# Optimization experiments

Measured on AMD Instinct MI355X. Metric: run time of the kernel, lower is better.

Reference implementation:

```python
import jax, jax.numpy as jnp
import numpy as np

N_NODES = 100000
N_EDGES = 1600000
D_IN = 128
D_OUT = 128
EPS = 1e-12  # torch F.normalize default eps


def setup_inputs() -> dict:
    key = jax.random.key(0)
    k1, k2, k3, k4, k5 = jax.random.split(key, 5)
    features = jax.random.normal(k1, (N_NODES, D_IN), dtype=jnp.float32)
    edge_src = jax.random.randint(k2, (N_EDGES,), 0, N_NODES, dtype=jnp.int64)
    edge_dst = jax.random.randint(k3, (N_EDGES,), 0, N_NODES, dtype=jnp.int64)
    node_mask = jnp.ones((N_NODES,), dtype=bool)
    W = jax.random.normal(k4, (D_OUT, D_IN), dtype=jnp.float32) * (1.0 / np.sqrt(D_IN))
    b = jax.random.normal(k5, (D_OUT,), dtype=jnp.float32) * 0.01
    return {"features": features, "edge_src": edge_src, "edge_dst": edge_dst,
            "node_mask": node_mask, "W": W, "b": b}


def reference(features, edge_src, edge_dst, node_mask, W, b):
    # Message passing: sum neighbor (src) features into each dst node.
    msgs = features[edge_src]                                   # [E, D_IN]
    agg = jax.ops.segment_sum(msgs, edge_dst, num_segments=features.shape[0])  # [N, D_IN]
    # Active nodes: h_N[node] = features[node] + sum(neighbors); inactive keep features.
    h_N = jnp.where(node_mask[:, None], features + agg, features)
    # F.normalize(h_N, dim=1): L2 normalize rows with eps clamp.
    norm = jnp.linalg.norm(h_N, axis=1, keepdims=True)
    h_norm = h_N / jnp.maximum(norm, EPS)
    # Linear layer.
    return h_norm @ W.T + b
```

## Files before the change

### kernel.cpp

```cpp
#include <hip/hip_runtime.h>

#define N_NODES 100000
#define D 128
#define N_EDGES 1600000
#define NBINS 3125
#define BCAP 1024
#define NCB 49
#define CCAP 40960
#define EPB1 1000
#define SLICE 2048
#define NSLICE 20
#define AST 136
#define LCAP 64
#define LST 68

typedef unsigned short u16;
typedef __attribute__((ext_vector_type(8))) short short8;
typedef __attribute__((ext_vector_type(8))) unsigned short ushort8;
typedef __attribute__((ext_vector_type(4))) float f32x4;

__device__ __forceinline__ u16 f2bf(float f) {
    union { float f; unsigned int i; } c;
    c.f = f;
    unsigned int r = c.i + 0x7FFFu + ((c.i >> 16) & 1u);
    return (u16)(r >> 16);
}

__device__ __forceinline__ void bf16_acc8(unsigned int u, float* a) {
    union { unsigned int i; float f; } c;
    c.i = u << 16;          a[0] += c.f;
    c.i = u & 0xffff0000u;  a[1] += c.f;
}

__global__ __launch_bounds__(256) void conv_all(const float* __restrict__ feat,
                                                const float* __restrict__ Wg,
                                                u16* __restrict__ featb,
                                                u16* __restrict__ Wbf,
                                                int* __restrict__ gcnt) {
    const int b = blockIdx.x, t = threadIdx.x;
    if (b < 6250) {
        if (!featb) return;
        int idx = (b * 256 + t) * 8;
        f32x4 v0 = *(const f32x4*)(feat + idx);
        f32x4 v1 = *(const f32x4*)(feat + idx + 4);
        ushort8 o;
        o[0] = f2bf(v0.x); o[1] = f2bf(v0.y); o[2] = f2bf(v0.z); o[3] = f2bf(v0.w);
        o[4] = f2bf(v1.x); o[5] = f2bf(v1.y); o[6] = f2bf(v1.z); o[7] = f2bf(v1.w);
        *(ushort8*)(featb + idx) = o;
    } else if (b < 6258) {
        int idx = ((b - 6250) * 256 + t) * 8;
        f32x4 v0 = *(const f32x4*)(Wg + idx);
        f32x4 v1 = *(const f32x4*)(Wg + idx + 4);
        ushort8 o;
        o[0] = f2bf(v0.x); o[1] = f2bf(v0.y); o[2] = f2bf(v0.z); o[3] = f2bf(v0.w);
        o[4] = f2bf(v1.x); o[5] = f2bf(v1.y); o[6] = f2bf(v1.z); o[7] = f2bf(v1.w);
        *(ushort8*)(Wbf + idx) = o;
    } else {
        int i = (b - 6258) * 256 + t;
        if (i < 3328) gcnt[i] = 0;
    }
}

__global__ __launch_bounds__(256) void coarse_bin(const int* __restrict__ esrc,
                                                  const int* __restrict__ edst,
                                                  int* __restrict__ gcnt,
                                                  int2* __restrict__ cpool) {
    __shared__ int2 stash[EPB1];
    __shared__ int hist[NCB];
    __shared__ int hbase[NCB];
    const int t = threadIdx.x;
    const int base = blockIdx.x * EPB1;

    if (t < NCB) hist[t] = 0;
    __syncthreads();
    for (int i = t; i < EPB1; i += 256) {
        int s = esrc[base + i];
        int d0 = edst[base + i];
        stash[i] = make_int2(s, d0);
        atomicAdd(&hist[d0 >> 11], 1);
    }
    __syncthreads();
    if (t < NCB) {
        int h = hist[t];
        hbase[t] = h ? atomicAdd(gcnt + 3136 + t, h) : 0;
        hist[t] = 0;
    }
    __syncthreads();
    for (int i = t; i < EPB1; i += 256) {
        int2 p = stash[i];
        int c = p.y >> 11;
        int r = atomicAdd(&hist[c], 1);
        int pos = hbase[c] + r;
        if (pos < CCAP) cpool[c * CCAP + pos] = p;
    }
}

__global__ __launch_bounds__(256) void fine_bin(int* __restrict__ gcnt,
                                                const int2* __restrict__ cpool,
                                                unsigned* __restrict__ pool) {
    __shared__ unsigned stash[SLICE];
    __shared__ unsigned char fwb[SLICE];
    __shared__ int hist[64];
    __shared__ int hbase[64];
    const int t = threadIdx.x;
    const int cb = blockIdx.x / NSLICE;
    const int sl = blockIdx.x % NSLICE;

    int cnt = gcnt[3136 + cb];
    if (cnt > CCAP) cnt = CCAP;
    int ne = cnt - sl * SLICE;
    if (ne <= 0) return;
    if (ne > SLICE) ne = SLICE;

    if (t < 64) hist[t] = 0;
    __syncthreads();
    const int2* seg = cpool + cb * CCAP + sl * SLICE;
    for (int i = t; i < ne; i += 256) {
        int2 p = seg[i];
        unsigned fw = ((unsigned)p.y >> 5) & 63u;
        stash[i] = ((unsigned)(p.y & 31) << 17) | (unsigned)p.x;
        fwb[i] = (unsigned char)fw;
        atomicAdd(&hist[fw], 1);
    }
    __syncthreads();
    if (t < 64) {
        int h = hist[t];
        hbase[t] = h ? atomicAdd(gcnt + cb * 64 + t, h) : 0;
        hist[t] = 0;
    }
    __syncthreads();
    for (int i = t; i < ne; i += 256) {
        int fw = fwb[i];
        int r = atomicAdd(&hist[fw], 1);
        int pos = hbase[fw] + r;
        if (pos < BCAP) pool[(size_t)(cb * 64 + fw) * BCAP + pos] = stash[i];
    }
}

template<bool BF16FEAT>
__global__ __launch_bounds__(256) void fused_gnl(const void* __restrict__ featv,
                                                 const int* __restrict__ gcnt,
                                                 const unsigned* __restrict__ pool,
                                                 const u16* __restrict__ Wbf,
                                                 const float* __restrict__ bg,
                                                 float* __restrict__ out) {
    __shared__ u16 Al[32 * AST];
    __shared__ int lists[32 * LST];
    __shared__ int lcnt[32];
    const int t = threadIdx.x;
    const int nbase = blockIdx.x * 32;
    const int nl = t >> 3;
    const int g = t & 7;
    const int n = nbase + nl;

    {
        int ne = gcnt[blockIdx.x];
        if (ne > BCAP) ne = BCAP;
        if (t < 32) lcnt[t] = 0;
        __syncthreads();
        const unsigned* seg = pool + (size_t)blockIdx.x * BCAP;
        for (int i = t; i < ne; i += 256) {
            unsigned p = seg[i];
            unsigned rel = p >> 17;
            int r = atomicAdd(&lcnt[rel], 1);
            if (r < LCAP) lists[rel * LST + r] = (int)(p & 0x1FFFFu);
        }
        __syncthreads();
    }

    float acc[16];
    if (BF16FEAT) {
        const u16* fb = (const u16*)featv + (size_t)n * D + g * 16;
        uint4 p0 = *(const uint4*)(fb);
        uint4 p1 = *(const uint4*)(fb + 8);
        #pragma unroll
        for (int k = 0; k < 16; k++) acc[k] = 0.f;
        bf16_acc8(p0.x, acc + 0);  bf16_acc8(p0.y, acc + 2);
        bf16_acc8(p0.z, acc + 4);  bf16_acc8(p0.w, acc + 6);
        bf16_acc8(p1.x, acc + 8);  bf16_acc8(p1.y, acc + 10);
        bf16_acc8(p1.z, acc + 12); bf16_acc8(p1.w, acc + 14);
    } else {
        const float* ff = (const float*)featv + (size_t)n * D + g * 16;
        f32x4 v0 = *(const f32x4*)(ff);
        f32x4 v1 = *(const f32x4*)(ff + 4);
        f32x4 v2 = *(const f32x4*)(ff + 8);
        f32x4 v3 = *(const f32x4*)(ff + 12);
        acc[0]=v0.x; acc[1]=v0.y; acc[2]=v0.z; acc[3]=v0.w;
        acc[4]=v1.x; acc[5]=v1.y; acc[6]=v1.z; acc[7]=v1.w;
        acc[8]=v2.x; acc[9]=v2.y; acc[10]=v2.z; acc[11]=v2.w;
        acc[12]=v3.x; acc[13]=v3.y; acc[14]=v3.z; acc[15]=v3.w;
    }

    int deg = lcnt[nl];
    if (deg > LCAP) deg = LCAP;
    const int* bk = lists + nl * LST;
    int e = 0;
    if (BF16FEAT) {
        const u16* fb = (const u16*)featv;
        for (; e + 4 <= deg; e += 4) {
            int4 s4 = *(const int4*)(bk + e);
            const u16* r0 = fb + (size_t)s4.x * D + g * 16;
            const u16* r1 = fb + (size_t)s4.y * D + g * 16;
            const u16* r2 = fb + (size_t)s4.z * D + g * 16;
            const u16* r3 = fb + (size_t)s4.w * D + g * 16;
            uint4 a0 = *(const uint4*)(r0), b0 = *(const uint4*)(r0 + 8);
            uint4 a1 = *(const uint4*)(r1), b1 = *(const uint4*)(r1 + 8);
            uint4 a2 = *(const uint4*)(r2), b2 = *(const uint4*)(r2 + 8);
            uint4 a3 = *(const uint4*)(r3), b3 = *(const uint4*)(r3 + 8);
            bf16_acc8(a0.x, acc+0); bf16_acc8(a0.y, acc+2); bf16_acc8(a0.z, acc+4); bf16_acc8(a0.w, acc+6);
            bf16_acc8(b0.x, acc+8); bf16_acc8(b0.y, acc+10); bf16_acc8(b0.z, acc+12); bf16_acc8(b0.w, acc+14);
            bf16_acc8(a1.x, acc+0); bf16_acc8(a1.y, acc+2); bf16_acc8(a1.z, acc+4); bf16_acc8(a1.w, acc+6);
            bf16_acc8(b1.x, acc+8); bf16_acc8(b1.y, acc+10); bf16_acc8(b1.z, acc+12); bf16_acc8(b1.w, acc+14);
            bf16_acc8(a2.x, acc+0); bf16_acc8(a2.y, acc+2); bf16_acc8(a2.z, acc+4); bf16_acc8(a2.w, acc+6);
            bf16_acc8(b2.x, acc+8); bf16_acc8(b2.y, acc+10); bf16_acc8(b2.z, acc+12); bf16_acc8(b2.w, acc+14);
            bf16_acc8(a3.x, acc+0); bf16_acc8(a3.y, acc+2); bf16_acc8(a3.z, acc+4); bf16_acc8(a3.w, acc+6);
            bf16_acc8(b3.x, acc+8); bf16_acc8(b3.y, acc+10); bf16_acc8(b3.z, acc+12); bf16_acc8(b3.w, acc+14);
        }
        for (; e < deg; e++) {
            const u16* r0 = fb + (size_t)bk[e] * D + g * 16;
            uint4 a0 = *(const uint4*)(r0), b0 = *(const uint4*)(r0 + 8);
            bf16_acc8(a0.x, acc+0); bf16_acc8(a0.y, acc+2); bf16_acc8(a0.z, acc+4); bf16_acc8(a0.w, acc+6);
            bf16_acc8(b0.x, acc+8); bf16_acc8(b0.y, acc+10); bf16_acc8(b0.z, acc+12); bf16_acc8(b0.w, acc+14);
        }
    } else {
        const float* ff = (const float*)featv;
        for (; e + 2 <= deg; e += 2) {
            int2 s2 = *(const int2*)(bk + e);
            const float* r0 = ff + (size_t)s2.x * D + g * 16;
            const float* r1 = ff + (size_t)s2.y * D + g * 16;
            f32x4 x0 = *(const f32x4*)(r0),     x1 = *(const f32x4*)(r0 + 4);
            f32x4 x2 = *(const f32x4*)(r0 + 8), x3 = *(const f32x4*)(r0 + 12);
            f32x4 y0 = *(const f32x4*)(r1),     y1 = *(const f32x4*)(r1 + 4);
            f32x4 y2 = *(const f32x4*)(r1 + 8), y3 = *(const f32x4*)(r1 + 12);
            acc[0]+=x0.x+y0.x; acc[1]+=x0.y+y0.y; acc[2]+=x0.z+y0.z; acc[3]+=x0.w+y0.w;
            acc[4]+=x1.x+y1.x; acc[5]+=x1.y+y1.y; acc[6]+=x1.z+y1.z; acc[7]+=x1.w+y1.w;
            acc[8]+=x2.x+y2.x; acc[9]+=x2.y+y2.y; acc[10]+=x2.z+y2.z; acc[11]+=x2.w+y2.w;
            acc[12]+=x3.x+y3.x; acc[13]+=x3.y+y3.y; acc[14]+=x3.z+y3.z; acc[15]+=x3.w+y3.w;
        }
        for (; e < deg; e++) {
            const float* r0 = ff + (size_t)bk[e] * D + g * 16;
            f32x4 x0 = *(const f32x4*)(r0),     x1 = *(const f32x4*)(r0 + 4);
            f32x4 x2 = *(const f32x4*)(r0 + 8), x3 = *(const f32x4*)(r0 + 12);
            acc[0]+=x0.x; acc[1]+=x0.y; acc[2]+=x0.z; acc[3]+=x0.w;
            acc[4]+=x1.x; acc[5]+=x1.y; acc[6]+=x1.z; acc[7]+=x1.w;
            acc[8]+=x2.x; acc[9]+=x2.y; acc[10]+=x2.z; acc[11]+=x2.w;
            acc[12]+=x3.x; acc[13]+=x3.y; acc[14]+=x3.z; acc[15]+=x3.w;
        }
    }

    float ss = 0.f;
    #pragma unroll
    for (int k = 0; k < 16; k++) ss += acc[k] * acc[k];
    #pragma unroll
    for (int off = 4; off; off >>= 1) ss += __shfl_xor(ss, off, 8);
    const float inv = 1.0f / fmaxf(sqrtf(ss), 1e-12f);

    {
        ushort8 o0, o1;
        o0[0]=f2bf(acc[0]*inv); o0[1]=f2bf(acc[1]*inv); o0[2]=f2bf(acc[2]*inv); o0[3]=f2bf(acc[3]*inv);
        o0[4]=f2bf(acc[4]*inv); o0[5]=f2bf(acc[5]*inv); o0[6]=f2bf(acc[6]*inv); o0[7]=f2bf(acc[7]*inv);
        o1[0]=f2bf(acc[8]*inv); o1[1]=f2bf(acc[9]*inv); o1[2]=f2bf(acc[10]*inv); o1[3]=f2bf(acc[11]*inv);
        o1[4]=f2bf(acc[12]*inv); o1[5]=f2bf(acc[13]*inv); o1[6]=f2bf(acc[14]*inv); o1[7]=f2bf(acc[15]*inv);
        u16* dst = Al + nl * AST + g * 16;
        *(ushort8*)(dst)     = o0;
        *(ushort8*)(dst + 8) = o1;
    }
    __syncthreads();

    const int w = t >> 6, lane = t & 63;
    const int mb = (w >> 1) * 16, nb = (w & 1) * 64;
    const int quad = lane >> 4, r = lane & 15;
    f32x4 c0 = {0,0,0,0}, c1 = {0,0,0,0}, c2 = {0,0,0,0}, c3 = {0,0,0,0};
    #pragma unroll
    for (int kt = 0; kt < 4; kt++) {
        const int ko = kt * 32 + quad * 8;
        short8 a  = *(const short8*)(Al + (mb + r) * AST + ko);
        short8 b0 = *(const short8*)(Wbf + (nb +  0 + r) * D + ko);
        short8 b1 = *(const short8*)(Wbf + (nb + 16 + r) * D + ko);
        short8 b2 = *(const short8*)(Wbf + (nb + 32 + r) * D + ko);
        short8 b3 = *(const short8*)(Wbf + (nb + 48 + r) * D + ko);
        c0 = __builtin_amdgcn_mfma_f32_16x16x32_bf16(a, b0, c0, 0, 0, 0);
        c1 = __builtin_amdgcn_mfma_f32_16x16x32_bf16(a, b1, c1, 0, 0, 0);
        c2 = __builtin_amdgcn_mfma_f32_16x16x32_bf16(a, b2, c2, 0, 0, 0);
        c3 = __builtin_amdgcn_mfma_f32_16x16x32_bf16(a, b3, c3, 0, 0, 0);
    }

    {
        const float bb0 = bg[nb + r], bb1 = bg[nb + 16 + r];
        const float bb2 = bg[nb + 32 + r], bb3 = bg[nb + 48 + r];
        float* outb = out + (size_t)(nbase + mb + quad * 4) * D;
        #pragma unroll
        for (int reg = 0; reg < 4; reg++) {
            float* rowp = outb + reg * D + nb + r;
            rowp[0]  = c0[reg] + bb0;
            rowp[16] = c1[reg] + bb1;
            rowp[32] = c2[reg] + bb2;
            rowp[48] = c3[reg] + bb3;
        }
    }
}

__global__ __launch_bounds__(256) void scatter(const float* __restrict__ feat,
                                               const int* __restrict__ esrc,
                                               const int* __restrict__ edst,
                                               float* __restrict__ agg) {
    int gid = blockIdx.x * 256 + threadIdx.x;
    int e = gid >> 5;
    int q = (gid & 31) << 2;
    int s = esrc[e];
    int d0 = edst[e];
    const float4 a = *(const float4*)(feat + s * D + q);
    float* dst = agg + d0 * D + q;
    unsafeAtomicAdd(dst + 0, a.x);
    unsafeAtomicAdd(dst + 1, a.y);
    unsafeAtomicAdd(dst + 2, a.z);
    unsafeAtomicAdd(dst + 3, a.w);
}

__global__ __launch_bounds__(256) void norm_linear_mfma(const float* __restrict__ Wg,
                                                        const float* __restrict__ bg,
                                                        float* __restrict__ out) {
    __shared__ u16 Wl[128 * AST];
    __shared__ u16 Al[32 * AST];
    __shared__ float bl[128];
    const int t = threadIdx.x;
    const int nbase = blockIdx.x * 32;

    for (int idx = t * 8; idx < 128 * 128; idx += 256 * 8) {
        int row = idx >> 7, col = idx & 127;
        f32x4 v0 = *(const f32x4*)(Wg + idx);
        f32x4 v1 = *(const f32x4*)(Wg + idx + 4);
        u16* dst = Wl + row * AST + col;
        dst[0] = f2bf(v0.x); dst[1] = f2bf(v0.y); dst[2] = f2bf(v0.z); dst[3] = f2bf(v0.w);
        dst[4] = f2bf(v1.x); dst[5] = f2bf(v1.y); dst[6] = f2bf(v1.z); dst[7] = f2bf(v1.w);
    }
    if (t < 128) bl[t] = bg[t];
    {
        const int n = t >> 3, seg = t & 7;
        const float* src = out + (nbase + n) * D + seg * 16;
        f32x4 v0 = *(const f32x4*)(src);
        f32x4 v1 = *(const f32x4*)(src + 4);
        f32x4 v2 = *(const f32x4*)(src + 8);
        f32x4 v3 = *(const f32x4*)(src + 12);
        float ss = v0.x*v0.x + v0.y*v0.y + v0.z*v0.z + v0.w*v0.w
                 + v1.x*v1.x + v1.y*v1.y + v1.z*v1.z + v1.w*v1.w
                 + v2.x*v2.x + v2.y*v2.y + v2.z*v2.z + v2.w*v2.w
                 + v3.x*v3.x + v3.y*v3.y + v3.z*v3.z + v3.w*v3.w;
        #pragma unroll
        for (int off = 4; off; off >>= 1) ss += __shfl_xor(ss, off, 8);
        const float inv = 1.0f / fmaxf(sqrtf(ss), 1e-12f);
        u16* dst = Al + n * AST + seg * 16;
        dst[0]  = f2bf(v0.x * inv); dst[1]  = f2bf(v0.y * inv);
        dst[2]  = f2bf(v0.z * inv); dst[3]  = f2bf(v0.w * inv);
        dst[4]  = f2bf(v1.x * inv); dst[5]  = f2bf(v1.y * inv);
        dst[6]  = f2bf(v1.z * inv); dst[7]  = f2bf(v1.w * inv);
        dst[8]  = f2bf(v2.x * inv); dst[9]  = f2bf(v2.y * inv);
        dst[10] = f2bf(v2.z * inv); dst[11] = f2bf(v2.w * inv);
        dst[12] = f2bf(v3.x * inv); dst[13] = f2bf(v3.y * inv);
        dst[14] = f2bf(v3.z * inv); dst[15] = f2bf(v3.w * inv);
    }
    __syncthreads();

    const int w = t >> 6, lane = t & 63;
    const int mb = (w >> 1) * 16, nb = (w & 1) * 64;
    const int quad = lane >> 4, r = lane & 15;
    f32x4 c0 = {0,0,0,0}, c1 = {0,0,0,0}, c2 = {0,0,0,0}, c3 = {0,0,0,0};
    #pragma unroll
    for (int kt = 0; kt < 4; kt++) {
        const int ko = kt * 32 + quad * 8;
        short8 a = *(const short8*)(Al + (mb + r) * AST + ko);
        short8 b0 = *(const short8*)(Wl + (nb +  0 + r) * AST + ko);
        short8 b1 = *(const short8*)(Wl + (nb + 16 + r) * AST + ko);
        short8 b2 = *(const short8*)(Wl + (nb + 32 + r) * AST + ko);
        short8 b3 = *(const short8*)(Wl + (nb + 48 + r) * AST + ko);
        c0 = __builtin_amdgcn_mfma_f32_16x16x32_bf16(a, b0, c0, 0, 0, 0);
        c1 = __builtin_amdgcn_mfma_f32_16x16x32_bf16(a, b1, c1, 0, 0, 0);
        c2 = __builtin_amdgcn_mfma_f32_16x16x32_bf16(a, b2, c2, 0, 0, 0);
        c3 = __builtin_amdgcn_mfma_f32_16x16x32_bf16(a, b3, c3, 0, 0, 0);
    }
    {
        float* outb = out + (nbase + mb + quad * 4) * D;
        const float bb0 = bl[nb + r], bb1 = bl[nb + 16 + r];
        const float bb2 = bl[nb + 32 + r], bb3 = bl[nb + 48 + r];
        #pragma unroll
        for (int reg = 0; reg < 4; reg++) {
            float* rowp = outb + reg * D + nb + r;
            rowp[0]  = c0[reg] + bb0;
            rowp[16] = c1[reg] + bb1;
            rowp[32] = c2[reg] + bb2;
            rowp[48] = c3[reg] + bb3;
        }
    }
}

extern "C" void kernel_launch(void* const* d_in, const int* in_sizes, int n_in,
                              void* d_out, int out_size, void* d_ws, size_t ws_size,
                              hipStream_t stream) {
    const float* feat = (const float*)d_in[0];
    const int*   esrc = (const int*)d_in[1];
    const int*   edst = (const int*)d_in[2];
    const float* W = (const float*)d_in[n_in - 2];
    const float* b = (const float*)d_in[n_in - 1];
    float* out = (float*)d_out;

    const long poolw = (long)NBINS * BCAP;
    const long need_f32  = 3328 + 8192 + poolw;
    const long need_bf16 = need_f32 + 6400000;
    const long availw = (long)(ws_size / 4);

    if (availw >= need_f32) {
        const bool bf16feat = (availw >= need_bf16);
        int* gcnt = (int*)d_ws;
        u16* Wbf = (u16*)(gcnt + 3328);
        unsigned* pool = (unsigned*)(Wbf + 16384);
        u16* featb = bf16feat ? (u16*)(pool + poolw) : (u16*)nullptr;
        int2* cpool = (int2*)d_out;

        conv_all<<<6271, 256, 0, stream>>>(feat, W, featb, Wbf, gcnt);
        coarse_bin<<<N_EDGES / EPB1, 256, 0, stream>>>(esrc, edst, gcnt, cpool);
        fine_bin<<<NCB * NSLICE, 256, 0, stream>>>(gcnt, cpool, pool);
        if (bf16feat)
            fused_gnl<true><<<NBINS, 256, 0, stream>>>(featb, gcnt, pool, Wbf, b, out);
        else
            fused_gnl<false><<<NBINS, 256, 0, stream>>>(feat, gcnt, pool, Wbf, b, out);
    } else {
        hipMemcpyAsync(out, feat, (size_t)N_NODES * D * sizeof(float),
                       hipMemcpyDeviceToDevice, stream);
        scatter<<<(N_EDGES * 32) / 256, 256, 0, stream>>>(feat, esrc, edst, out);
        norm_linear_mfma<<<N_NODES / 32, 256, 0, stream>>>(W, b, out);
    }
}
```

Baseline: 235.1 us.

## Halve fused-kernel node tile to 16 and split neighbor gather across thread pairs

The fused gather/normalize/linear kernel now handles 16 nodes per block instead of 32. Each node gets 16 threads, with two threads splitting the neighbor quads and combining their partial sums through a shuffle. Fine binning goes to 128 bins per coarse bin with a bucket capacity of 512, and coarse_bin first sorts edges locally in shared memory so its global writes are contiguous. The aim is more blocks and more memory-level parallelism in the gather, and better coalescing in binning. The cost is an extra shuffle reduction, a smaller MFMA tile per block, and W fragments being reloaded by twice as many blocks.

```diff
diff --git a/kernel.cpp b/kernel.cpp
--- a/kernel.cpp
+++ b/kernel.cpp
@@ -3,8 +3,9 @@
 #define N_NODES 100000
 #define D 128
 #define N_EDGES 1600000
-#define NBINS 3125
-#define BCAP 1024
+#define NBINS 6250
+#define BCAP 512
+#define NFINW 6272
 #define NCB 49
 #define CCAP 40960
 #define EPB1 1000
@@ -57,7 +58,7 @@
         *(ushort8*)(Wbf + idx) = o;
     } else {
         int i = (b - 6258) * 256 + t;
-        if (i < 3328) gcnt[i] = 0;
+        if (i < 6400) gcnt[i] = 0;
     }
 }
 
@@ -66,8 +67,10 @@
                                                   int* __restrict__ gcnt,
                                                   int2* __restrict__ cpool) {
     __shared__ int2 stash[EPB1];
+    __shared__ int2 sorted[EPB1];
     __shared__ int hist[NCB];
     __shared__ int hbase[NCB];
+    __shared__ int loff[NCB];
     const int t = threadIdx.x;
     const int base = blockIdx.x * EPB1;
 
@@ -80,9 +83,14 @@
         atomicAdd(&hist[d0 >> 11], 1);
     }
     __syncthreads();
+    if (t == 0) {
+        int run = 0;
+        for (int c = 0; c < NCB; c++) { loff[c] = run; run += hist[c]; }
+    }
+    __syncthreads();
     if (t < NCB) {
         int h = hist[t];
-        hbase[t] = h ? atomicAdd(gcnt + 3136 + t, h) : 0;
+        hbase[t] = h ? atomicAdd(gcnt + NFINW + t, h) : 0;
         hist[t] = 0;
     }
     __syncthreads();
@@ -90,7 +98,13 @@
         int2 p = stash[i];
         int c = p.y >> 11;
         int r = atomicAdd(&hist[c], 1);
-        int pos = hbase[c] + r;
+        sorted[loff[c] + r] = p;
+    }
+    __syncthreads();
+    for (int i = t; i < EPB1; i += 256) {
+        int2 p = sorted[i];
+        int c = p.y >> 11;
+        int pos = hbase[c] + (i - loff[c]);
         if (pos < CCAP) cpool[c * CCAP + pos] = p;
     }
 }
@@ -100,32 +114,32 @@
                                                 unsigned* __restrict__ pool) {
     __shared__ unsigned stash[SLICE];
     __shared__ unsigned char fwb[SLICE];
-    __shared__ int hist[64];
-    __shared__ int hbase[64];
+    __shared__ int hist[128];
+    __shared__ int hbase[128];
     const int t = threadIdx.x;
     const int cb = blockIdx.x / NSLICE;
     const int sl = blockIdx.x % NSLICE;
 
-    int cnt = gcnt[3136 + cb];
+    int cnt = gcnt[NFINW + cb];
     if (cnt > CCAP) cnt = CCAP;
     int ne = cnt - sl * SLICE;
     if (ne <= 0) return;
     if (ne > SLICE) ne = SLICE;
 
-    if (t < 64) hist[t] = 0;
+    if (t < 128) hist[t] = 0;
     __syncthreads();
     const int2* seg = cpool + cb * CCAP + sl * SLICE;
     for (int i = t; i < ne; i += 256) {
         int2 p = seg[i];
-        unsigned fw = ((unsigned)p.y >> 5) & 63u;
-        stash[i] = ((unsigned)(p.y & 31) << 17) | (unsigned)p.x;
+        unsigned fw = ((unsigned)p.y >> 4) & 127u;
+        stash[i] = ((unsigned)(p.y & 15) << 17) | (unsigned)p.x;
         fwb[i] = (unsigned char)fw;
         atomicAdd(&hist[fw], 1);
     }
     __syncthreads();
-    if (t < 64) {
+    if (t < 128) {
         int h = hist[t];
-        hbase[t] = h ? atomicAdd(gcnt + cb * 64 + t, h) : 0;
+        hbase[t] = h ? atomicAdd(gcnt + cb * 128 + t, h) : 0;
         hist[t] = 0;
     }
     __syncthreads();
@@ -133,7 +147,7 @@
         int fw = fwb[i];
         int r = atomicAdd(&hist[fw], 1);
         int pos = hbase[fw] + r;
-        if (pos < BCAP) pool[(size_t)(cb * 64 + fw) * BCAP + pos] = stash[i];
+        if (pos < BCAP) pool[(size_t)(cb * 128 + fw) * BCAP + pos] = stash[i];
     }
 }
 
@@ -144,19 +158,20 @@
                                                  const u16* __restrict__ Wbf,
                                                  const float* __restrict__ bg,
                                                  float* __restrict__ out) {
-    __shared__ u16 Al[32 * AST];
-    __shared__ int lists[32 * LST];
-    __shared__ int lcnt[32];
+    __shared__ u16 Al[16 * AST];
+    __shared__ int lists[16 * LST];
+    __shared__ int lcnt[16];
     const int t = threadIdx.x;
-    const int nbase = blockIdx.x * 32;
-    const int nl = t >> 3;
-    const int g = t & 7;
+    const int nbase = blockIdx.x * 16;
+    const int nl = t >> 4;
+    const int g = (t >> 1) & 7;
+    const int h = t & 1;
     const int n = nbase + nl;
 
     {
         int ne = gcnt[blockIdx.x];
         if (ne > BCAP) ne = BCAP;
-        if (t < 32) lcnt[t] = 0;
+        if (t < 16) lcnt[t] = 0;
         __syncthreads();
         const unsigned* seg = pool + (size_t)blockIdx.x * BCAP;
         for (int i = t; i < ne; i += 256) {
@@ -169,36 +184,40 @@
     }
 
     float acc[16];
+    #pragma unroll
+    for (int k = 0; k < 16; k++) acc[k] = 0.f;
     if (BF16FEAT) {
-        const u16* fb = (const u16*)featv + (size_t)n * D + g * 16;
-        uint4 p0 = *(const uint4*)(fb);
-        uint4 p1 = *(const uint4*)(fb + 8);
-        #pragma unroll
-        for (int k = 0; k < 16; k++) acc[k] = 0.f;
-        bf16_acc8(p0.x, acc + 0);  bf16_acc8(p0.y, acc + 2);
-        bf16_acc8(p0.z, acc + 4);  bf16_acc8(p0.w, acc + 6);
-        bf16_acc8(p1.x, acc + 8);  bf16_acc8(p1.y, acc + 10);
-        bf16_acc8(p1.z, acc + 12); bf16_acc8(p1.w, acc + 14);
+        if (h == 0) {
+            const u16* fr = (const u16*)featv + (size_t)n * D + g * 16;
+            uint4 p0 = *(const uint4*)(fr);
+            uint4 p1 = *(const uint4*)(fr + 8);
+            bf16_acc8(p0.x, acc + 0);  bf16_acc8(p0.y, acc + 2);
+            bf16_acc8(p0.z, acc + 4);  bf16_acc8(p0.w, acc + 6);
+            bf16_acc8(p1.x, acc + 8);  bf16_acc8(p1.y, acc + 10);
+            bf16_acc8(p1.z, acc + 12); bf16_acc8(p1.w, acc + 14);
+        }
     } else {
-        const float* ff = (const float*)featv + (size_t)n * D + g * 16;
-        f32x4 v0 = *(const f32x4*)(ff);
-        f32x4 v1 = *(const f32x4*)(ff + 4);
-        f32x4 v2 = *(const f32x4*)(ff + 8);
-        f32x4 v3 = *(const f32x4*)(ff + 12);
-        acc[0]=v0.x; acc[1]=v0.y; acc[2]=v0.z; acc[3]=v0.w;
-        acc[4]=v1.x; acc[5]=v1.y; acc[6]=v1.z; acc[7]=v1.w;
-        acc[8]=v2.x; acc[9]=v2.y; acc[10]=v2.z; acc[11]=v2.w;
-        acc[12]=v3.x; acc[13]=v3.y; acc[14]=v3.z; acc[15]=v3.w;
+        if (h == 0) {
+            const float* ff = (const float*)featv + (size_t)n * D + g * 16;
+            f32x4 v0 = *(const f32x4*)(ff);
+            f32x4 v1 = *(const f32x4*)(ff + 4);
+            f32x4 v2 = *(const f32x4*)(ff + 8);
+            f32x4 v3 = *(const f32x4*)(ff + 12);
+            acc[0]=v0.x; acc[1]=v0.y; acc[2]=v0.z; acc[3]=v0.w;
+            acc[4]=v1.x; acc[5]=v1.y; acc[6]=v1.z; acc[7]=v1.w;
+            acc[8]=v2.x; acc[9]=v2.y; acc[10]=v2.z; acc[11]=v2.w;
+            acc[12]=v3.x; acc[13]=v3.y; acc[14]=v3.z; acc[15]=v3.w;
+        }
     }
 
     int deg = lcnt[nl];
     if (deg > LCAP) deg = LCAP;
     const int* bk = lists + nl * LST;
-    int e = 0;
+    const int m4 = deg >> 2;
     if (BF16FEAT) {
         const u16* fb = (const u16*)featv;
-        for (; e + 4 <= deg; e += 4) {
-            int4 s4 = *(const int4*)(bk + e);
+        for (int q = h; q < m4; q += 2) {
+            int4 s4 = *(const int4*)(bk + q * 4);
             const u16* r0 = fb + (size_t)s4.x * D + g * 16;
             const u16* r1 = fb + (size_t)s4.y * D + g * 16;
             const u16* r2 = fb + (size_t)s4.z * D + g * 16;
@@ -216,46 +235,55 @@
             bf16_acc8(a3.x, acc+0); bf16_acc8(a3.y, acc+2); bf16_acc8(a3.z, acc+4); bf16_acc8(a3.w, acc+6);
             bf16_acc8(b3.x, acc+8); bf16_acc8(b3.y, acc+10); bf16_acc8(b3.z, acc+12); bf16_acc8(b3.w, acc+14);
         }
-        for (; e < deg; e++) {
-            const u16* r0 = fb + (size_t)bk[e] * D + g * 16;
-            uint4 a0 = *(const uint4*)(r0), b0 = *(const uint4*)(r0 + 8);
-            bf16_acc8(a0.x, acc+0); bf16_acc8(a0.y, acc+2); bf16_acc8(a0.z, acc+4); bf16_acc8(a0.w, acc+6);
-            bf16_acc8(b0.x, acc+8); bf16_acc8(b0.y, acc+10); bf16_acc8(b0.z, acc+12); bf16_acc8(b0.w, acc+14);
+        if (h == (m4 & 1)) {
+            for (int e = m4 * 4; e < deg; e++) {
+                const u16* r0 = fb + (size_t)bk[e] * D + g * 16;
+                uint4 a0 = *(const uint4*)(r0), b0 = *(const uint4*)(r0 + 8);
+                bf16_acc8(a0.x, acc+0); bf16_acc8(a0.y, acc+2); bf16_acc8(a0.z, acc+4); bf16_acc8(a0.w, acc+6);
+                bf16_acc8(b0.x, acc+8); bf16_acc8(b0.y, acc+10); bf16_acc8(b0.z, acc+12); bf16_acc8(b0.w, acc+14);
+            }
         }
     } else {
         const float* ff = (const float*)featv;
-        for (; e + 2 <= deg; e += 2) {
-            int2 s2 = *(const int2*)(bk + e);
-            const float* r0 = ff + (size_t)s2.x * D + g * 16;
-            const float* r1 = ff + (size_t)s2.y * D + g * 16;
-            f32x4 x0 = *(const f32x4*)(r0),     x1 = *(const f32x4*)(r0 + 4);
-            f32x4 x2 = *(const f32x4*)(r0 + 8), x3 = *(const f32x4*)(r0 + 12);
-            f32x4 y0 = *(const f32x4*)(r1),     y1 = *(const f32x4*)(r1 + 4);
-            f32x4 y2 = *(const f32x4*)(r1 + 8), y3 = *(const f32x4*)(r1 + 12);
-            acc[0]+=x0.x+y0.x; acc[1]+=x0.y+y0.y; acc[2]+=x0.z+y0.z; acc[3]+=x0.w+y0.w;
-            acc[4]+=x1.x+y1.x; acc[5]+=x1.y+y1.y; acc[6]+=x1.z+y1.z; acc[7]+=x1.w+y1.w;
-            acc[8]+=x2.x+y2.x; acc[9]+=x2.y+y2.y; acc[10]+=x2.z+y2.z; acc[11]+=x2.w+y2.w;
-            acc[12]+=x3.x+y3.x; acc[13]+=x3.y+y3.y; acc[14]+=x3.z+y3.z; acc[15]+=x3.w+y3.w;
-        }
-        for (; e < deg; e++) {
-            const float* r0 = ff + (size_t)bk[e] * D + g * 16;
-            f32x4 x0 = *(const f32x4*)(r0),     x1 = *(const f32x4*)(r0 + 4);
-            f32x4 x2 = *(const f32x4*)(r0 + 8), x3 = *(const f32x4*)(r0 + 12);
-            acc[0]+=x0.x; acc[1]+=x0.y; acc[2]+=x0.z; acc[3]+=x0.w;
-            acc[4]+=x1.x; acc[5]+=x1.y; acc[6]+=x1.z; acc[7]+=x1.w;
-            acc[8]+=x2.x; acc[9]+=x2.y; acc[10]+=x2.z; acc[11]+=x2.w;
-            acc[12]+=x3.x; acc[13]+=x3.y; acc[14]+=x3.z; acc[15]+=x3.w;
-        }
-    }
+        for (int q = h; q < m4; q += 2) {
+            int4 s4 = *(const int4*)(bk + q * 4);
+            #pragma unroll
+            for (int j = 0; j < 4; j++) {
+                int sidx = (j == 0) ? s4.x : (j == 1) ? s4.y : (j == 2) ? s4.z : s4.w;
+                const float* r0 = ff + (size_t)sidx * D + g * 16;
+                f32x4 x0 = *(const f32x4*)(r0),     x1 = *(const f32x4*)(r0 + 4);
+                f32x4 x2 = *(const f32x4*)(r0 + 8), x3 = *(const f32x4*)(r0 + 12);
+                acc[0]+=x0.x; acc[1]+=x0.y; acc[2]+=x0.z; acc[3]+=x0.w;
+                acc[4]+=x1.x; acc[5]+=x1.y; acc[6]+=x1.z; acc[7]+=x1.w;
+                acc[8]+=x2.x; acc[9]+=x2.y; acc[10]+=x2.z; acc[11]+=x2.w;
+                acc[12]+=x3.x; acc[13]+=x3.y; acc[14]+=x3.z; acc[15]+=x3.w;
+            }
+        }
+        if (h == (m4 & 1)) {
+            for (int e = m4 * 4; e < deg; e++) {
+                const float* r0 = ff + (size_t)bk[e] * D + g * 16;
+                f32x4 x0 = *(const f32x4*)(r0),     x1 = *(const f32x4*)(r0 + 4);
+                f32x4 x2 = *(const f32x4*)(r0 + 8), x3 = *(const f32x4*)(r0 + 12);
+                acc[0]+=x0.x; acc[1]+=x0.y; acc[2]+=x0.z; acc[3]+=x0.w;
+                acc[4]+=x1.x; acc[5]+=x1.y; acc[6]+=x1.z; acc[7]+=x1.w;
+                acc[8]+=x2.x; acc[9]+=x2.y; acc[10]+=x2.z; acc[11]+=x2.w;
+                acc[12]+=x3.x; acc[13]+=x3.y; acc[14]+=x3.z; acc[15]+=x3.w;
+            }
+        }
+    }
+
+    #pragma unroll
+    for (int k = 0; k < 16; k++) acc[k] += __shfl_xor(acc[k], 1);
 
     float ss = 0.f;
     #pragma unroll
     for (int k = 0; k < 16; k++) ss += acc[k] * acc[k];
-    #pragma unroll
-    for (int off = 4; off; off >>= 1) ss += __shfl_xor(ss, off, 8);
+    ss += __shfl_xor(ss, 2, 16);
+    ss += __shfl_xor(ss, 4, 16);
+    ss += __shfl_xor(ss, 8, 16);
     const float inv = 1.0f / fmaxf(sqrtf(ss), 1e-12f);
 
-    {
+    if (h == 0) {
         ushort8 o0, o1;
         o0[0]=f2bf(acc[0]*inv); o0[1]=f2bf(acc[1]*inv); o0[2]=f2bf(acc[2]*inv); o0[3]=f2bf(acc[3]*inv);
         o0[4]=f2bf(acc[4]*inv); o0[5]=f2bf(acc[5]*inv); o0[6]=f2bf(acc[6]*inv); o0[7]=f2bf(acc[7]*inv);
@@ -268,34 +296,26 @@
     __syncthreads();
 
     const int w = t >> 6, lane = t & 63;
-    const int mb = (w >> 1) * 16, nb = (w & 1) * 64;
+    const int nb = w * 32;
     const int quad = lane >> 4, r = lane & 15;
-    f32x4 c0 = {0,0,0,0}, c1 = {0,0,0,0}, c2 = {0,0,0,0}, c3 = {0,0,0,0};
+    f32x4 c0 = {0,0,0,0}, c1 = {0,0,0,0};
     #pragma unroll
     for (int kt = 0; kt < 4; kt++) {
         const int ko = kt * 32 + quad * 8;
-        short8 a  = *(const short8*)(Al + (mb + r) * AST + ko);
+        short8 a  = *(const short8*)(Al + r * AST + ko);
         short8 b0 = *(const short8*)(Wbf + (nb +  0 + r) * D + ko);
         short8 b1 = *(const short8*)(Wbf + (nb + 16 + r) * D + ko);
-        short8 b2 = *(const short8*)(Wbf + (nb + 32 + r) * D + ko);
-        short8 b3 = *(const short8*)(Wbf + (nb + 48 + r) * D + ko);
         c0 = __builtin_amdgcn_mfma_f32_16x16x32_bf16(a, b0, c0, 0, 0, 0);
         c1 = __builtin_amdgcn_mfma_f32_16x16x32_bf16(a, b1, c1, 0, 0, 0);
-        c2 = __builtin_amdgcn_mfma_f32_16x16x32_bf16(a, b2, c2, 0, 0, 0);
-        c3 = __builtin_amdgcn_mfma_f32_16x16x32_bf16(a, b3, c3, 0, 0, 0);
-    }
-
+    }
     {
         const float bb0 = bg[nb + r], bb1 = bg[nb + 16 + r];
-        const float bb2 = bg[nb + 32 + r], bb3 = bg[nb + 48 + r];
-        float* outb = out + (size_t)(nbase + mb + quad * 4) * D;
+        float* outb = out + (size_t)(nbase + quad * 4) * D;
         #pragma unroll
         for (int reg = 0; reg < 4; reg++) {
             float* rowp = outb + reg * D + nb + r;
             rowp[0]  = c0[reg] + bb0;
             rowp[16] = c1[reg] + bb1;
-            rowp[32] = c2[reg] + bb2;
-            rowp[48] = c3[reg] + bb3;
         }
     }
 }
@@ -403,20 +423,20 @@
     const float* b = (const float*)d_in[n_in - 1];
     float* out = (float*)d_out;
 
-    const long poolw = (long)NBINS * BCAP;
-    const long need_f32  = 3328 + 8192 + poolw;
+    const long poolw = (long)NFINW * BCAP;
+    const long need_f32  = 6400 + 8192 + poolw;
     const long need_bf16 = need_f32 + 6400000;
     const long availw = (long)(ws_size / 4);
 
     if (availw >= need_f32) {
         const bool bf16feat = (availw >= need_bf16);
         int* gcnt = (int*)d_ws;
-        u16* Wbf = (u16*)(gcnt + 3328);
+        u16* Wbf = (u16*)(gcnt + 6400);
         unsigned* pool = (unsigned*)(Wbf + 16384);
         u16* featb = bf16feat ? (u16*)(pool + poolw) : (u16*)nullptr;
         int2* cpool = (int2*)d_out;
 
-        conv_all<<<6271, 256, 0, stream>>>(feat, W, featb, Wbf, gcnt);
+        conv_all<<<6283, 256, 0, stream>>>(feat, W, featb, Wbf, gcnt);
         coarse_bin<<<N_EDGES / EPB1, 256, 0, stream>>>(esrc, edst, gcnt, cpool);
         fine_bin<<<NCB * NSLICE, 256, 0, stream>>>(gcnt, cpool, pool);
         if (bf16feat)
```

Result: no change. 234.0 us (-0.5%).
